# Kernel optimization log

Hardware: AMD Instinct MI355X
Metric: run time of the kernel (lower is better)

The kernel has to match this reference:

```python
import jax, jax.numpy as jnp
import numpy as np

NUM_AXES = 72
NUM_PARAMS = 12
D_MODEL = 1024
SEQ_LEN = 4096
MAX_PROP = 600
LN_EPS = 1e-5


def setup_inputs() -> dict:
    key = jax.random.key(0)
    k1, k2, k3 = jax.random.split(key, 3)
    hidden_states = jax.random.normal(k1, (1, SEQ_LEN, D_MODEL), dtype=jnp.float32)
    ln_gamma = jnp.ones((D_MODEL,), dtype=jnp.float32)
    ln_beta = jnp.zeros((D_MODEL,), dtype=jnp.float32)
    W = jax.random.normal(k2, (NUM_AXES * NUM_PARAMS, D_MODEL), dtype=jnp.float32) * (1.0 / np.sqrt(D_MODEL))
    b = jax.random.normal(k3, (NUM_AXES * NUM_PARAMS,), dtype=jnp.float32) * 0.02
    return {"hidden_states": hidden_states, "ln_gamma": ln_gamma, "ln_beta": ln_beta, "W": W, "b": b}


def reference(hidden_states, ln_gamma, ln_beta, W, b):
    S = hidden_states.shape[1]
    T = min(MAX_PROP, S)
    x = hidden_states[0]  # (S, D)
    # LayerNorm
    mu = jnp.mean(x, axis=-1, keepdims=True)
    var = jnp.mean((x - mu) ** 2, axis=-1, keepdims=True)
    h = (x - mu) * jax.lax.rsqrt(var + LN_EPS) * ln_gamma + ln_beta
    # Linear -> (S, 12, 72)
    p = (h @ W.T + b).reshape(S, NUM_PARAMS, NUM_AXES)
    sp = jax.nn.softplus
    c = p[:, 4]; c_th = p[:, 5]; phi = p[:, 6]; phi_th = p[:, 7]  # (S, A)
    d = sp(p[:, 1]); k = d * d / 4.0 + sp(p[:, 0])
    d_th = sp(p[:, 3]); k_th = d_th * d_th / 4.0 + sp(p[:, 2])
    omega1 = jnp.sqrt(4.0 * k - d * d) / 2.0
    omega1_th = jnp.sqrt(4.0 * k_th - d_th * d_th) / 2.0
    t = jnp.arange(T, dtype=jnp.float32)[None, :, None]  # (1, T, 1)
    # damped sinusoids, (S, T, A)
    lin = c[:, None, :] * jnp.exp(-d[:, None, :] / 2.0 * t) * jnp.sin(omega1[:, None, :] * t + phi[:, None, :])
    ang = c_th[:, None, :] * jnp.exp(-d_th[:, None, :] / 2.0 * t) * jnp.sin(omega1_th[:, None, :] * t + phi_th[:, None, :])
    sig = lin + ang
    # overlap-add: out[pos] += sig[s, t] where pos = s + t, keep pos < S
    pos = (jnp.arange(S)[:, None] + jnp.arange(T)[None, :]).reshape(-1)  # (S*T,)
    vals = sig.reshape(-1, NUM_AXES)
    vals = jnp.where((pos < S)[:, None], vals, 0.0)
    pos_c = jnp.minimum(pos, S - 1)
    summed = jax.ops.segment_sum(vals, pos_c, num_segments=S).T  # (A, S)
    acc_base = p[:, 8].T
    acc_std = sp(p[:, 9]).T
    gyro_base = p[:, 10].T
    gyro_std = sp(p[:, 11]).T
    return (summed, acc_base, acc_std, gyro_base, gyro_std)
```

## Files before the change

### kernel.cpp

```cpp
#include <hip/hip_runtime.h>
#include <hip/hip_bf16.h>
#include <math.h>

#define S_LEN   4096
#define DMODEL  1024
#define NAX     72
#define NPAR    12
#define NCOL    864
#define NCOLP   896
#define TPROP   600
#define LN_EPS  1e-5f
#define EPS_CUT 5e-7f

typedef _Float16 half4 __attribute__((ext_vector_type(4)));
typedef _Float16 half8 __attribute__((ext_vector_type(8)));
typedef float    f32x4  __attribute__((ext_vector_type(4)));
typedef float    f32x2  __attribute__((ext_vector_type(2)));
typedef float    f32x16 __attribute__((ext_vector_type(16)));

#define GLOAD16(gp, lp)                                                        \
    __builtin_amdgcn_global_load_lds(                                          \
        (const __attribute__((address_space(1))) void*)(gp),                   \
        (__attribute__((address_space(3))) void*)(lp), 16, 0, 0)

__global__ __launch_bounds__(256) void k_lnw(
    const float* __restrict__ x, const float* __restrict__ gamma,
    const float* __restrict__ beta, const float* __restrict__ W,
    _Float16* __restrict__ h, _Float16* __restrict__ Wf)
{
    int tid = threadIdx.x;
    if (blockIdx.x >= S_LEN) {
        int t = (blockIdx.x - S_LEN) * 256 + tid;
        int row = t >> 7;
        int c0  = (t & 127) * 8;
        half8 o;
        if (row < NCOL) {
            const float4* p = (const float4*)(W + (size_t)row * DMODEL + c0);
            float4 a = p[0], b = p[1];
            o[0]=(_Float16)a.x; o[1]=(_Float16)a.y; o[2]=(_Float16)a.z; o[3]=(_Float16)a.w;
            o[4]=(_Float16)b.x; o[5]=(_Float16)b.y; o[6]=(_Float16)b.z; o[7]=(_Float16)b.w;
        } else {
            #pragma unroll
            for (int i = 0; i < 8; ++i) o[i] = (_Float16)0.f;
        }
        *(half8*)(Wf + (size_t)row * DMODEL + c0) = o;
        return;
    }
    int row = blockIdx.x;
    const float4* xr = (const float4*)(x + (size_t)row * DMODEL);
    float4 v = xr[tid];
    float s  = v.x + v.y + v.z + v.w;
    float sq = v.x*v.x + v.y*v.y + v.z*v.z + v.w*v.w;
    #pragma unroll
    for (int off = 1; off < 64; off <<= 1) {
        s  += __shfl_xor(s, off);
        sq += __shfl_xor(sq, off);
    }
    __shared__ float ls[4], lq[4];
    int wid = tid >> 6, lane = tid & 63;
    if (lane == 0) { ls[wid] = s; lq[wid] = sq; }
    __syncthreads();
    s  = ls[0] + ls[1] + ls[2] + ls[3];
    sq = lq[0] + lq[1] + lq[2] + lq[3];
    float mu  = s * (1.f / DMODEL);
    float var = sq * (1.f / DMODEL) - mu * mu;
    float rs  = rsqrtf(var + LN_EPS);
    float4 g = ((const float4*)gamma)[tid];
    float4 b = ((const float4*)beta)[tid];
    half4 o;
    o.x = (_Float16)((v.x - mu) * rs * g.x + b.x);
    o.y = (_Float16)((v.y - mu) * rs * g.y + b.y);
    o.z = (_Float16)((v.z - mu) * rs * g.z + b.z);
    o.w = (_Float16)((v.w - mu) * rs * g.w + b.w);
    ((half4*)(h + (size_t)row * DMODEL))[tid] = o;
}

__global__ __launch_bounds__(256) void k_gemm(
    const _Float16* __restrict__ A, const _Float16* __restrict__ B,
    const float* __restrict__ bias, float* __restrict__ P)
{
    __shared__ char smem[12288];
    char* smA = smem;
    char* smB = smem + 8192;

    int tid  = threadIdx.x;
    int lane = tid & 63;
    int wid  = tid >> 6;
    int wr   = wid >> 1, wc = wid & 1;
    int n0   = blockIdx.x * 64;
    int m0   = blockIdx.y * 128;

    int qa0 = tid, qa1 = tid + 256;
    int ar0 = qa0 >> 2, ac0 = (qa0 & 3) ^ ((ar0 >> 1) & 3);
    int ar1 = qa1 >> 2, ac1 = (qa1 & 3) ^ ((ar1 >> 1) & 3);
    int br  = tid >> 2, bc  = (tid & 3) ^ ((br >> 1) & 3);
    const _Float16* gA0 = A + (size_t)(m0 + ar0) * DMODEL + ac0 * 8;
    const _Float16* gA1 = A + (size_t)(m0 + ar1) * DMODEL + ac1 * 8;
    const _Float16* gB  = B + (size_t)(n0 + br)  * DMODEL + bc  * 8;

    int fr  = lane & 15;
    int chs = ((lane >> 4) ^ ((lane >> 1) & 3)) * 16;
    int aoff[4], boff[2];
    #pragma unroll
    for (int m = 0; m < 4; ++m) aoff[m] = (wr * 64 + m * 16 + fr) * 64 + chs;
    #pragma unroll
    for (int n = 0; n < 2; ++n) boff[n] = (wc * 32 + n * 16 + fr) * 64 + chs;

    f32x4 acc[4][2];
    #pragma unroll
    for (int m = 0; m < 4; ++m)
        #pragma unroll
        for (int n = 0; n < 2; ++n) acc[m][n] = (f32x4){0.f, 0.f, 0.f, 0.f};

    for (int k0 = 0; k0 < DMODEL; k0 += 32) {
        if (k0) __syncthreads();
        GLOAD16(gA0 + k0, smA + qa0 * 16);
        GLOAD16(gA1 + k0, smA + qa1 * 16);
        GLOAD16(gB  + k0, smB + tid * 16);
        __syncthreads();

        half8 af[4], bf[2];
        #pragma unroll
        for (int m = 0; m < 4; ++m) af[m] = *(const half8*)(smA + aoff[m]);
        #pragma unroll
        for (int n = 0; n < 2; ++n) bf[n] = *(const half8*)(smB + boff[n]);
        #pragma unroll
        for (int m = 0; m < 4; ++m)
            #pragma unroll
            for (int n = 0; n < 2; ++n)
                acc[m][n] = __builtin_amdgcn_mfma_f32_16x16x32_f16(
                                af[m], bf[n], acc[m][n], 0, 0, 0);
    }

    int rb = m0 + wr * 64 + (lane >> 4) * 4;
    #pragma unroll
    for (int n = 0; n < 2; ++n) {
        int col = n0 + wc * 32 + n * 16 + fr;
        float bv = (col < NCOL) ? bias[col] : 0.f;
        #pragma unroll
        for (int m = 0; m < 4; ++m) {
            int r0 = rb + m * 16;
            #pragma unroll
            for (int j = 0; j < 4; ++j)
                P[(size_t)(r0 + j) * NCOLP + col] = acc[m][n][j] + bv;
        }
    }
}

__device__ __forceinline__ float softplus_f(float x) {
    return fmaxf(x, 0.f) + log1pf(expf(-fabsf(x)));
}

__global__ __launch_bounds__(256) void k_params(
    float* __restrict__ P, float* __restrict__ params,
    float* __restrict__ out)
{
    int g = blockIdx.x * 256 + threadIdx.x;
    if (g >= S_LEN * NAX) return;
    int s = g / NAX, a = g - s * NAX;
    const float* pr = P + (size_t)s * NCOLP + a;
    float p0  = pr[0*NAX], p1  = pr[1*NAX], p2  = pr[2*NAX], p3  = pr[3*NAX];
    float p4  = pr[4*NAX], p5  = pr[5*NAX], p6  = pr[6*NAX], p7  = pr[7*NAX];
    float p8  = pr[8*NAX], p9  = pr[9*NAX], p10 = pr[10*NAX], p11 = pr[11*NAX];

    float d  = softplus_f(p1), hd  = 0.5f * d;
    float w  = sqrtf(softplus_f(p0));
    float A  = 2.f * expf(-hd) * cosf(w);
    float B  = expf(-d);
    float d2 = softplus_f(p3), hd2 = 0.5f * d2;
    float w2 = sqrtf(softplus_f(p2));
    float A2 = 2.f * expf(-hd2) * cosf(w2);
    float B2 = expf(-d2);

    float4* pp = (float4*)(params + ((size_t)a * S_LEN + s) * 12);
    pp[0] = make_float4(A,   A2,  B,   B2);
    pp[1] = make_float4(p4,  p5,  hd,  hd2);
    pp[2] = make_float4(w,   w2,  p6,  p7);

    float tl = __logf(fabsf(p4) * (1.f / EPS_CUT)) / hd;
    float ta = __logf(fabsf(p5) * (1.f / EPS_CUT)) / hd2;
    float tm = fmaxf(tl, ta);
    tm = fminf(tm, 599.f);
    tm = fmaxf(tm, 0.f);
    int tm8 = (((int)tm + 8) >> 3);
    if (tm8 > 255) tm8 = 255;
    ((unsigned char*)P)[(size_t)s * (NCOLP * 4) + NCOL * 4 + a] = (unsigned char)tm8;

    size_t o1 = (size_t)NAX * S_LEN;
    float* o = out + (size_t)a * S_LEN + s;
    o[1*o1] = p8;
    o[2*o1] = softplus_f(p9);
    o[3*o1] = p10;
    o[4*o1] = softplus_f(p11);
}

__device__ __forceinline__ f32x2 sin2(f32x2 v) {
    f32x2 r; r.x = __sinf(v.x); r.y = __sinf(v.y); return r;
}
__device__ __forceinline__ f32x2 exp2e(f32x2 v) {
    f32x2 r; r.x = __expf(v.x); r.y = __expf(v.y); return r;
}

#define PK_MUL_IP(d, s)                                                        \
    asm("v_pk_mul_f32 %0, %1, %0" : "+v"(d) : "v"(s))
#define PK_FMA_IP(d, a, b)                                                     \
    asm("v_pk_fma_f32 %0, %1, %2, %0" : "+v"(d) : "v"(a), "v"(b))

#define OSTEP2(V,K,KB) do {                                                    \
    PK_MUL_IP(xa, nB2v); PK_FMA_IP(xa, A2v, xb);  V[K]   += xa.x + xa.y;       \
    PK_MUL_IP(xb, nB2v); PK_FMA_IP(xb, A2v, xa);  V[K+1] += xb.x + xb.y; } while(0)

#define OSTEP2M(V,K,KB) do {                                                   \
    PK_MUL_IP(xa, nB2v); PK_FMA_IP(xa, A2v, xb);                               \
    V[K]   += (((KB)+(K))   <= iLim) ? (xa.x + xa.y) : 0.f;                    \
    PK_MUL_IP(xb, nB2v); PK_FMA_IP(xb, A2v, xa);                               \
    V[K+1] += (((KB)+(K)+1) <= iLim) ? (xb.x + xb.y) : 0.f; } while(0)

#define OSTEP2S(V,K,KB) do {                                                   \
    bool c0 = (((KB)+(K)) == lane);                                            \
    PK_MUL_IP(xa, nB2v); PK_FMA_IP(xa, A2v, xb);                               \
    xa.x = c0 ? x0.x : xa.x;   xa.y = c0 ? x0.y : xa.y;                        \
    xb.x = c0 ? xm1.x : xb.x;  xb.y = c0 ? xm1.y : xb.y;                       \
    V[K] += xa.x + xa.y;                                                       \
    bool c1 = (((KB)+(K)+1) == lane);                                          \
    PK_MUL_IP(xb, nB2v); PK_FMA_IP(xb, A2v, xa);                               \
    xb.x = c1 ? x0.x : xb.x;   xb.y = c1 ? x0.y : xb.y;                        \
    xa.x = c1 ? xm1.x : xa.x;  xa.y = c1 ? xm1.y : xa.y;                       \
    V[K+1] += xb.x + xb.y; } while(0)

#define RUN4P(OP)                                                              \
    { _Pragma("unroll") for (int k2=0;k2<8;++k2) OP(acc0,2*k2,0);              \
      _Pragma("unroll") for (int k2=0;k2<8;++k2) OP(acc1,2*k2,16);             \
      _Pragma("unroll") for (int k2=0;k2<8;++k2) OP(acc2,2*k2,32);             \
      _Pragma("unroll") for (int k2=0;k2<8;++k2) OP(acc3,2*k2,48); }

#define LOADP(J, Q0, Q1, Q2) do {                                              \
    int tb_ = ((J) - 1) * 64 + 1 + lane;                                       \
    int s_  = P0 - tb_;                                                        \
    int sc_ = (s_ >= 0 && tb_ <= 599) ? s_ : 0;                                \
    const float4* pp_ = (const float4*)(pbase + (size_t)sc_ * 12);             \
    Q0 = pp_[0]; Q1 = pp_[1]; Q2 = pp_[2]; } while(0)

__global__ __launch_bounds__(128, 3) void k_scan(
    const float* __restrict__ params, const float* __restrict__ Pm,
    float* __restrict__ out)
{
    __shared__ unsigned short tbuf[2][576];
    int tid  = threadIdx.x;
    int lane = tid & 63;
    int wid  = tid >> 6;
    int g    = (blockIdx.x & 7) * 288 + (blockIdx.x >> 3);
    int a    = g >> 5;
    int p    = g & 31;
    int tile = wid ? (63 - p) : p;
    int P0   = tile << 6;
    int nb   = tile < 10 ? tile : 10;

    f32x16 acc0 = {}, acc1 = {}, acc2 = {}, acc3 = {};

    const float* pbase = params + (size_t)a * S_LEN * 12;
    const unsigned char* tmax8 = (const unsigned char*)Pm;

    float4 n0, n1, n2;

    {
        int s = P0 + lane;
        const float4* pp = (const float4*)(pbase + (size_t)s * 12);
        float4 q0 = pp[0], q1 = pp[1], q2 = pp[2];
        if (nb >= 1) LOADP(1, n0, n1, n2);
        f32x2 A2v = {q0.x, q0.y};
        f32x2 nB2v = {-q0.z, -q0.w};
        f32x2 c2  = {q1.x, q1.y};
        f32x2 w2v = {q2.x, q2.y}, ph2 = {q2.z, q2.w};
        f32x2 ehd; ehd.x = rsqrtf(-nB2v.x); ehd.y = rsqrtf(-nB2v.y);
        f32x2 x0  = c2 * sin2(ph2);
        f32x2 xm1 = c2 * ehd * sin2(ph2 - w2v);
        f32x2 xa = {0.f, 0.f}, xb = {0.f, 0.f};
        RUN4P(OSTEP2S)
    }

    if (nb >= 1) {
        float4 q0 = n0, q1 = n1, q2 = n2;
        int tb = lane + 1;
        f32x2 A2v = {q0.x, q0.y};
        f32x2 nB2v = {-q0.z, -q0.w};
        f32x2 c2  = {q1.x, q1.y}, hd2 = {q1.z, q1.w};
        f32x2 w2v = {q2.x, q2.y}, ph2 = {q2.z, q2.w};
        f32x2 ehd; ehd.x = rsqrtf(-nB2v.x); ehd.y = rsqrtf(-nB2v.y);
        float fu = (float)(tb - 1);
        f32x2 e2 = c2 * exp2e(-hd2 * fu);

        bool alive = (fabsf(e2.x) > EPS_CUT) || (fabsf(e2.y) > EPS_CUT);
        if (__ballot(alive) != 0ULL) {
            f32x2 s1 = w2v * fu + ph2;
            f32x2 xb = e2 * sin2(s1);
            f32x2 xa = e2 * ehd * sin2(s1 - w2v);
            RUN4P(OSTEP2)
        }
    }

    if (nb >= 2) {
        int nA = 0;
        for (int j = 2; j <= nb; ++j) {
            int tb = (j - 1) * 64 + 1 + lane;
            bool alive = false;
            if (tb <= 599) {
                unsigned char t8 = tmax8[(size_t)(P0 - tb) * (NCOLP * 4) + NCOL * 4 + a];
                alive = (tb >> 3) <= (int)t8;
            }
            unsigned long long m = __ballot(alive);
            if (alive) {
                int rank = __popcll(m & ((1ULL << lane) - 1ULL));
                tbuf[wid][nA + rank] = (unsigned short)tb;
            }
            nA += (int)__popcll(m);
        }
        __builtin_amdgcn_wave_barrier();

        for (int base = 0; base < nA; base += 64) {
            int idx = base + lane;
            bool act = idx < nA;
            int tb = act ? (int)tbuf[wid][idx] : 1;
            const float4* pp = (const float4*)(pbase + (size_t)(P0 - tb) * 12);
            float4 q0 = pp[0], q1 = pp[1], q2 = pp[2];
            f32x2 A2v = {q0.x, q0.y};
            f32x2 nB2v = {-q0.z, -q0.w};
            f32x2 c2  = {q1.x, q1.y}, hd2 = {q1.z, q1.w};
            f32x2 w2v = {q2.x, q2.y}, ph2 = {q2.z, q2.w};
            if (!act) { c2.x = 0.f; c2.y = 0.f; }
            f32x2 ehd; ehd.x = rsqrtf(-nB2v.x); ehd.y = rsqrtf(-nB2v.y);
            float fu = (float)(tb - 1);
            f32x2 e2 = c2 * exp2e(-hd2 * fu);
            f32x2 s1 = w2v * fu + ph2;
            f32x2 xb = e2 * sin2(s1);
            f32x2 xa = e2 * ehd * sin2(s1 - w2v);
            int iLim = 599 - tb;
            RUN4P(OSTEP2M)
        }
    }

    bool s32 = (lane & 32) != 0;
    #pragma unroll
    for (int k = 0; k < 16; ++k) {
        float keep = s32 ? acc2[k] : acc0[k];
        float send = s32 ? acc0[k] : acc2[k];
        acc0[k] = keep + __shfl_xor(send, 32);
    }
    #pragma unroll
    for (int k = 0; k < 16; ++k) {
        float keep = s32 ? acc3[k] : acc1[k];
        float send = s32 ? acc1[k] : acc3[k];
        acc1[k] = keep + __shfl_xor(send, 32);
    }
    bool s16 = (lane & 16) != 0;
    #pragma unroll
    for (int k = 0; k < 16; ++k) {
        float keep = s16 ? acc1[k] : acc0[k];
        float send = s16 ? acc0[k] : acc1[k];
        acc0[k] = keep + __shfl_xor(send, 16);
    }
    bool s8 = (lane & 8) != 0;
    #pragma unroll
    for (int k = 0; k < 8; ++k) {
        float keep = s8 ? acc0[k + 8] : acc0[k];
        float send = s8 ? acc0[k]     : acc0[k + 8];
        acc0[k] = keep + __shfl_xor(send, 8);
    }
    bool s4 = (lane & 4) != 0;
    #pragma unroll
    for (int k = 0; k < 4; ++k) {
        float keep = s4 ? acc0[k + 4] : acc0[k];
        float send = s4 ? acc0[k]     : acc0[k + 4];
        acc0[k] = keep + __shfl_xor(send, 4);
    }
    bool s2 = (lane & 2) != 0;
    #pragma unroll
    for (int k = 0; k < 2; ++k) {
        float keep = s2 ? acc0[k + 2] : acc0[k];
        float send = s2 ? acc0[k]     : acc0[k + 2];
        acc0[k] = keep + __shfl_xor(send, 2);
    }
    bool s1 = (lane & 1) != 0;
    {
        float keep = s1 ? acc0[1] : acc0[0];
        float send = s1 ? acc0[0] : acc0[1];
        acc0[0] = keep + __shfl_xor(send, 1);
    }
    out[(size_t)a * S_LEN + P0 + lane] = acc0[0];
}

extern "C" void kernel_launch(void* const* d_in, const int* in_sizes, int n_in,
                              void* d_out, int out_size, void* d_ws, size_t ws_size,
                              hipStream_t stream)
{
    const float* x     = (const float*)d_in[0];
    const float* gamma = (const float*)d_in[1];
    const float* beta  = (const float*)d_in[2];
    const float* W     = (const float*)d_in[3];
    const float* bias  = (const float*)d_in[4];
    float* out = (float*)d_out;

    const size_t P_BYTES = (size_t)S_LEN * NCOLP * 4;
    char* ws = (char*)d_ws;
    float*    Pm     = (float*)ws;
    float*    params = (float*)(ws + P_BYTES);
    _Float16* hf     = (_Float16*)(ws + P_BYTES);
    _Float16* Wf     = (_Float16*)(ws + P_BYTES + (size_t)S_LEN * DMODEL * 2);

    k_lnw<<<dim3(S_LEN + NCOLP / 2), dim3(256), 0, stream>>>(x, gamma, beta, W, hf, Wf);
    k_gemm<<<dim3(NCOLP / 64, S_LEN / 128), dim3(256), 0, stream>>>(hf, Wf, bias, Pm);
    k_params<<<dim3((S_LEN * NAX + 255) / 256), dim3(256), 0, stream>>>(Pm, params, out);
    k_scan<<<dim3(2304), dim3(128), 0, stream>>>(params, Pm, out);
}
```

Before: 69.03 us.

## Split each scan tile across two waves and store tmax in compact per-axis array

The scan kernel now assigns one output tile per block and splits the work inside it: wave 0 handles the self and first-neighbour segments, and wave 1 handles the far contributions selected by the alive test. The two partial sums are combined through shared memory, which doubles the grid to 4608 blocks. The per-position tmax byte moves from a strided slot inside the P matrix to a contiguous axis-major array, so the alive scan reads nearby bytes and all nine checks can be issued up front. The intra-block split may be unbalanced, and it adds a barrier and an extra shared-memory exchange.

```diff
diff --git a/kernel.cpp b/kernel.cpp
--- a/kernel.cpp
+++ b/kernel.cpp
@@ -152,8 +152,8 @@
 }
 
 __global__ __launch_bounds__(256) void k_params(
-    float* __restrict__ P, float* __restrict__ params,
-    float* __restrict__ out)
+    const float* __restrict__ P, float* __restrict__ params,
+    unsigned char* __restrict__ tmax8, float* __restrict__ out)
 {
     int g = blockIdx.x * 256 + threadIdx.x;
     if (g >= S_LEN * NAX) return;
@@ -184,7 +184,7 @@
     tm = fmaxf(tm, 0.f);
     int tm8 = (((int)tm + 8) >> 3);
     if (tm8 > 255) tm8 = 255;
-    ((unsigned char*)P)[(size_t)s * (NCOLP * 4) + NCOL * 4 + a] = (unsigned char)tm8;
+    tmax8[(size_t)a * S_LEN + s] = (unsigned char)tm8;
 
     size_t o1 = (size_t)NAX * S_LEN;
     float* o = out + (size_t)a * S_LEN + s;
@@ -222,7 +222,7 @@
     xa.x = c0 ? x0.x : xa.x;   xa.y = c0 ? x0.y : xa.y;                        \
     xb.x = c0 ? xm1.x : xb.x;  xb.y = c0 ? xm1.y : xb.y;                       \
     V[K] += xa.x + xa.y;                                                       \
-    bool c1 = (((KB)+(K)+1) == lane);                                          \
+    bool c1 = (((K)+(KB)+1) == lane);                                          \
     PK_MUL_IP(xb, nB2v); PK_FMA_IP(xb, A2v, xa);                               \
     xb.x = c1 ? x0.x : xb.x;   xb.y = c1 ? x0.y : xb.y;                        \
     xa.x = c1 ? xm1.x : xa.x;  xa.y = c1 ? xm1.y : xa.y;                       \
@@ -234,84 +234,82 @@
       _Pragma("unroll") for (int k2=0;k2<8;++k2) OP(acc2,2*k2,32);             \
       _Pragma("unroll") for (int k2=0;k2<8;++k2) OP(acc3,2*k2,48); }
 
-#define LOADP(J, Q0, Q1, Q2) do {                                              \
-    int tb_ = ((J) - 1) * 64 + 1 + lane;                                       \
-    int s_  = P0 - tb_;                                                        \
-    int sc_ = (s_ >= 0 && tb_ <= 599) ? s_ : 0;                                \
-    const float4* pp_ = (const float4*)(pbase + (size_t)sc_ * 12);             \
-    Q0 = pp_[0]; Q1 = pp_[1]; Q2 = pp_[2]; } while(0)
-
 __global__ __launch_bounds__(128, 3) void k_scan(
-    const float* __restrict__ params, const float* __restrict__ Pm,
+    const float* __restrict__ params, const unsigned char* __restrict__ tmax8,
     float* __restrict__ out)
 {
-    __shared__ unsigned short tbuf[2][576];
+    __shared__ unsigned short tbuf[576];
+    __shared__ float xch[64];
     int tid  = threadIdx.x;
     int lane = tid & 63;
     int wid  = tid >> 6;
-    int g    = (blockIdx.x & 7) * 288 + (blockIdx.x >> 3);
-    int a    = g >> 5;
-    int p    = g & 31;
-    int tile = wid ? (63 - p) : p;
+    int g    = (blockIdx.x & 7) * 576 + (blockIdx.x >> 3);
+    int a    = g >> 6;
+    int tile = g & 63;
     int P0   = tile << 6;
     int nb   = tile < 10 ? tile : 10;
 
     f32x16 acc0 = {}, acc1 = {}, acc2 = {}, acc3 = {};
 
     const float* pbase = params + (size_t)a * S_LEN * 12;
-    const unsigned char* tmax8 = (const unsigned char*)Pm;
-
-    float4 n0, n1, n2;
-
-    {
-        int s = P0 + lane;
-        const float4* pp = (const float4*)(pbase + (size_t)s * 12);
-        float4 q0 = pp[0], q1 = pp[1], q2 = pp[2];
-        if (nb >= 1) LOADP(1, n0, n1, n2);
-        f32x2 A2v = {q0.x, q0.y};
-        f32x2 nB2v = {-q0.z, -q0.w};
-        f32x2 c2  = {q1.x, q1.y};
-        f32x2 w2v = {q2.x, q2.y}, ph2 = {q2.z, q2.w};
-        f32x2 ehd; ehd.x = rsqrtf(-nB2v.x); ehd.y = rsqrtf(-nB2v.y);
-        f32x2 x0  = c2 * sin2(ph2);
-        f32x2 xm1 = c2 * ehd * sin2(ph2 - w2v);
-        f32x2 xa = {0.f, 0.f}, xb = {0.f, 0.f};
-        RUN4P(OSTEP2S)
-    }
-
-    if (nb >= 1) {
-        float4 q0 = n0, q1 = n1, q2 = n2;
-        int tb = lane + 1;
-        f32x2 A2v = {q0.x, q0.y};
-        f32x2 nB2v = {-q0.z, -q0.w};
-        f32x2 c2  = {q1.x, q1.y}, hd2 = {q1.z, q1.w};
-        f32x2 w2v = {q2.x, q2.y}, ph2 = {q2.z, q2.w};
-        f32x2 ehd; ehd.x = rsqrtf(-nB2v.x); ehd.y = rsqrtf(-nB2v.y);
-        float fu = (float)(tb - 1);
-        f32x2 e2 = c2 * exp2e(-hd2 * fu);
-
-        bool alive = (fabsf(e2.x) > EPS_CUT) || (fabsf(e2.y) > EPS_CUT);
-        if (__ballot(alive) != 0ULL) {
-            f32x2 s1 = w2v * fu + ph2;
-            f32x2 xb = e2 * sin2(s1);
-            f32x2 xa = e2 * ehd * sin2(s1 - w2v);
-            RUN4P(OSTEP2)
-        }
-    }
-
-    if (nb >= 2) {
+
+    if (wid == 0) {
+        float4 n0, n1, n2;
+        {
+            int s = P0 + lane;
+            const float4* pp = (const float4*)(pbase + (size_t)s * 12);
+            float4 q0 = pp[0], q1 = pp[1], q2 = pp[2];
+            if (nb >= 1) {
+                int tb_ = 1 + lane;
+                const float4* pp_ = (const float4*)(pbase + (size_t)(P0 - tb_) * 12);
+                n0 = pp_[0]; n1 = pp_[1]; n2 = pp_[2];
+            }
+            f32x2 A2v = {q0.x, q0.y};
+            f32x2 nB2v = {-q0.z, -q0.w};
+            f32x2 c2  = {q1.x, q1.y};
+            f32x2 w2v = {q2.x, q2.y}, ph2 = {q2.z, q2.w};
+            f32x2 ehd; ehd.x = rsqrtf(-nB2v.x); ehd.y = rsqrtf(-nB2v.y);
+            f32x2 x0  = c2 * sin2(ph2);
+            f32x2 xm1 = c2 * ehd * sin2(ph2 - w2v);
+            f32x2 xa = {0.f, 0.f}, xb = {0.f, 0.f};
+            RUN4P(OSTEP2S)
+        }
+        if (nb >= 1) {
+            float4 q0 = n0, q1 = n1, q2 = n2;
+            int tb = lane + 1;
+            f32x2 A2v = {q0.x, q0.y};
+            f32x2 nB2v = {-q0.z, -q0.w};
+            f32x2 c2  = {q1.x, q1.y}, hd2 = {q1.z, q1.w};
+            f32x2 w2v = {q2.x, q2.y}, ph2 = {q2.z, q2.w};
+            f32x2 ehd; ehd.x = rsqrtf(-nB2v.x); ehd.y = rsqrtf(-nB2v.y);
+            float fu = (float)(tb - 1);
+            f32x2 e2 = c2 * exp2e(-hd2 * fu);
+            bool alive = (fabsf(e2.x) > EPS_CUT) || (fabsf(e2.y) > EPS_CUT);
+            if (__ballot(alive) != 0ULL) {
+                f32x2 s1 = w2v * fu + ph2;
+                f32x2 xb = e2 * sin2(s1);
+                f32x2 xa = e2 * ehd * sin2(s1 - w2v);
+                RUN4P(OSTEP2)
+            }
+        }
+    } else if (nb >= 2) {
+        const unsigned char* tma = tmax8 + (size_t)a * S_LEN;
+        bool alv[9];
+        #pragma unroll
+        for (int jj = 0; jj < 9; ++jj) {
+            int j  = jj + 2;
+            int tb = (j - 1) * 64 + 1 + lane;
+            bool okt = (j <= nb) && (tb <= 599);
+            unsigned char t8 = okt ? tma[P0 - tb] : (unsigned char)0;
+            alv[jj] = okt && ((tb >> 3) <= (int)t8);
+        }
         int nA = 0;
-        for (int j = 2; j <= nb; ++j) {
-            int tb = (j - 1) * 64 + 1 + lane;
-            bool alive = false;
-            if (tb <= 599) {
-                unsigned char t8 = tmax8[(size_t)(P0 - tb) * (NCOLP * 4) + NCOL * 4 + a];
-                alive = (tb >> 3) <= (int)t8;
-            }
-            unsigned long long m = __ballot(alive);
-            if (alive) {
+        #pragma unroll
+        for (int jj = 0; jj < 9; ++jj) {
+            unsigned long long m = __ballot(alv[jj]);
+            if (alv[jj]) {
                 int rank = __popcll(m & ((1ULL << lane) - 1ULL));
-                tbuf[wid][nA + rank] = (unsigned short)tb;
+                tbuf[nA + rank] = (unsigned short)((jj + 1) * 64 + 1 + lane);
             }
             nA += (int)__popcll(m);
         }
@@ -320,7 +318,7 @@
         for (int base = 0; base < nA; base += 64) {
             int idx = base + lane;
             bool act = idx < nA;
-            int tb = act ? (int)tbuf[wid][idx] : 1;
+            int tb = act ? (int)tbuf[idx] : 1;
             const float4* pp = (const float4*)(pbase + (size_t)(P0 - tb) * 12);
             float4 q0 = pp[0], q1 = pp[1], q2 = pp[2];
             f32x2 A2v = {q0.x, q0.y};
@@ -386,7 +384,11 @@
         float send = s1 ? acc0[0] : acc0[1];
         acc0[0] = keep + __shfl_xor(send, 1);
     }
-    out[(size_t)a * S_LEN + P0 + lane] = acc0[0];
+
+    if (wid == 1) xch[lane] = acc0[0];
+    __syncthreads();
+    if (wid == 0)
+        out[(size_t)a * S_LEN + P0 + lane] = acc0[0] + xch[lane];
 }
 
 extern "C" void kernel_launch(void* const* d_in, const int* in_sizes, int n_in,
@@ -400,15 +402,17 @@
     const float* bias  = (const float*)d_in[4];
     float* out = (float*)d_out;
 
-    const size_t P_BYTES = (size_t)S_LEN * NCOLP * 4;
+    const size_t P_BYTES   = (size_t)S_LEN * NCOLP * 4;
+    const size_t PAR_BYTES = (size_t)S_LEN * NAX * 12 * 4;
     char* ws = (char*)d_ws;
-    float*    Pm     = (float*)ws;
-    float*    params = (float*)(ws + P_BYTES);
-    _Float16* hf     = (_Float16*)(ws + P_BYTES);
-    _Float16* Wf     = (_Float16*)(ws + P_BYTES + (size_t)S_LEN * DMODEL * 2);
+    float*         Pm     = (float*)ws;
+    float*         params = (float*)(ws + P_BYTES);
+    unsigned char* tmax8  = (unsigned char*)(ws + P_BYTES + PAR_BYTES);
+    _Float16*      hf     = (_Float16*)(ws + P_BYTES);
+    _Float16*      Wf     = (_Float16*)(ws + P_BYTES + (size_t)S_LEN * DMODEL * 2);
 
     k_lnw<<<dim3(S_LEN + NCOLP / 2), dim3(256), 0, stream>>>(x, gamma, beta, W, hf, Wf);
     k_gemm<<<dim3(NCOLP / 64, S_LEN / 128), dim3(256), 0, stream>>>(hf, Wf, bias, Pm);
-    k_params<<<dim3((S_LEN * NAX + 255) / 256), dim3(256), 0, stream>>>(Pm, params, out);
-    k_scan<<<dim3(2304), dim3(128), 0, stream>>>(params, Pm, out);
-}
+    k_params<<<dim3((S_LEN * NAX + 255) / 256), dim3(256), 0, stream>>>(Pm, params, tmax8, out);
+    k_scan<<<dim3(4608), dim3(128), 0, stream>>>(params, tmax8, out);
+}
```

New measurement: 70.33 us. Within noise of the previous version (+1.9%).
